# Kernel tuning notes

Measured on AMD Instinct MI355X. Metric: run time of the kernel, lower is better.

The kernel has to match this reference:

```python
import jax, jax.numpy as jnp
import numpy as np

N_MEL = 80; ARNN = 1024; ADIM = 128; EMB = 512; PRE = 256; DRNN = 1024; NF = 32; KS = 31
B = 32; NCTX = 512; T = 500
PAD = (KS - 1) // 2


def setup_inputs() -> dict:
    key = jax.random.key(0)
    ks = jax.random.split(key, 20)
    g = lambda k, shape: jax.random.normal(k, shape, dtype=jnp.float32) * 0.02
    return {
        "memory": jax.random.normal(ks[0], (B, NCTX, EMB), dtype=jnp.float32),
        "decoder_inputs": jax.random.normal(ks[1], (B, N_MEL, T), dtype=jnp.float32),
        "mask": jnp.zeros((B, NCTX), dtype=bool),
        "prenet_w1": g(ks[2], (PRE, N_MEL)),
        "prenet_w2": g(ks[3], (PRE, PRE)),
        "arnn_wih": g(ks[4], (4 * ARNN, PRE + EMB)),
        "arnn_whh": g(ks[5], (4 * ARNN, ARNN)),
        "arnn_bih": jnp.zeros((4 * ARNN,), jnp.float32),
        "arnn_bhh": jnp.zeros((4 * ARNN,), jnp.float32),
        "q_w": g(ks[6], (ADIM, ARNN)),
        "m_w": g(ks[7], (ADIM, EMB)),
        "loc_conv_w": g(ks[8], (NF, 2, KS)),
        "loc_w": g(ks[9], (ADIM, NF)),
        "v_w": g(ks[10], (ADIM,)),
        "drnn_wih": g(ks[11], (4 * DRNN, ARNN + EMB)),
        "drnn_whh": g(ks[12], (4 * DRNN, DRNN)),
        "drnn_bih": jnp.zeros((4 * DRNN,), jnp.float32),
        "drnn_bhh": jnp.zeros((4 * DRNN,), jnp.float32),
        "proj_w": g(ks[13], (N_MEL, DRNN + EMB)),
        "proj_b": jnp.zeros((N_MEL,), jnp.float32),
        "gate_w": g(ks[14], (1, DRNN + EMB)),
        "gate_b": jnp.zeros((1,), jnp.float32),
    }


def _lstm_cell(x, h, c, wih, whh, bih, bhh):
    # PyTorch LSTMCell gate order: i, f, g, o
    z = x @ wih.T + h @ whh.T + bih + bhh
    i, f, g, o = jnp.split(z, 4, axis=-1)
    c2 = jax.nn.sigmoid(f) * c + jax.nn.sigmoid(i) * jnp.tanh(g)
    h2 = jax.nn.sigmoid(o) * jnp.tanh(c2)
    return h2, c2


def reference(memory, decoder_inputs, mask,
              prenet_w1, prenet_w2,
              arnn_wih, arnn_whh, arnn_bih, arnn_bhh,
              q_w, m_w, loc_conv_w, loc_w, v_w,
              drnn_wih, drnn_whh, drnn_bih, drnn_bhh,
              proj_w, proj_b, gate_w, gate_b):
    b, n_ctx, emb = memory.shape
    n_mel, t_out = decoder_inputs.shape[1], decoder_inputs.shape[2]

    # (time, batch, n_mel) with a leading zero go-frame; PreNet (eval: no dropout)
    x = jnp.transpose(decoder_inputs, (2, 0, 1))
    x = jnp.concatenate([jnp.zeros((1, b, n_mel), x.dtype), x], axis=0)
    h = jax.nn.relu(x @ prenet_w1.T)
    h = jax.nn.relu(h @ prenet_w2.T)  # (T+1, B, PRE)
    inputs = h[:-1]  # T decoder steps

    proc_mem = memory @ m_w.T  # (B, n_ctx, ADIM)

    def step(carry, xin):
        ah, ac, dh, dc, aw, awc, actx = carry
        cell_in = jnp.concatenate([xin, actx], axis=-1)
        ah, ac = _lstm_cell(cell_in, ah, ac, arnn_wih, arnn_whh, arnn_bih, arnn_bhh)
        # location-sensitive attention
        aw_cat = jnp.stack([aw, awc], axis=1)  # (B, 2, n_ctx)
        loc = jax.lax.conv_general_dilated(
            aw_cat, loc_conv_w, window_strides=(1,), padding=[(PAD, PAD)],
            dimension_numbers=("NCH", "OIH", "NCH"))  # (B, NF, n_ctx)
        loc = jnp.transpose(loc, (0, 2, 1)) @ loc_w.T  # (B, n_ctx, ADIM)
        q = (ah @ q_w.T)[:, None, :]  # (B, 1, ADIM)
        e = jnp.tanh(q + proc_mem + loc) @ v_w  # (B, n_ctx)
        e = jnp.where(mask, -1e9, e)
        aw = jax.nn.softmax(e, axis=-1)
        actx = jnp.einsum("bn,bne->be", aw, memory)
        awc = awc + aw
        din = jnp.concatenate([ah, actx], axis=-1)
        dh, dc = _lstm_cell(din, dh, dc, drnn_wih, drnn_whh, drnn_bih, drnn_bhh)
        dhc = jnp.concatenate([dh, actx], axis=-1)
        mel = dhc @ proj_w.T + proj_b  # (B, n_mel)
        gate = dhc @ gate_w.T + gate_b  # (B, 1)
        return (ah, ac, dh, dc, aw, awc, actx), (mel, gate[:, 0])

    z32 = lambda *s: jnp.zeros(s, memory.dtype)
    carry0 = (z32(b, ARNN), z32(b, ARNN), z32(b, DRNN), z32(b, DRNN),
              z32(b, n_ctx), z32(b, n_ctx), z32(b, emb))
    _, (mels, gates) = jax.lax.scan(step, carry0, inputs)
    mel_out = jnp.transpose(mels, (1, 2, 0))   # (B, n_mel, T)
    gate_out = jnp.transpose(gates, (1, 0))    # (B, T)
    return mel_out, gate_out
```

## Files before the change

kernel.cpp:

```cpp
#include <hip/hip_runtime.h>

#define NBLK 256
#define NTHR 1024

constexpr int kNMel = 80, kArnn = 1024, kAdim = 128, kEmb = 512, kPre = 256;
constexpr int kNF = 32, kKS = 31, kB = 32, kNctx = 512, kT = 500, kPad = 15;

constexpr int KT_A = 56;
constexpr int KT_D = 80;
constexpr int KT_ALL = KT_A + KT_D;

constexpr int OFF_PREB   = 0;
constexpr int OFF_PROCMB = OFF_PREB + kT * kB * kPre / 2;
constexpr int OFF_QWTB   = OFF_PROCMB + kB * kNctx * kAdim / 2;
constexpr int OFF_LWT    = OFF_QWTB + kAdim * kArnn / 2;
constexpr int OFF_STATE  = OFF_LWT + kAdim * 33;
constexpr int OFF_AHB    = OFF_STATE;
constexpr int OFF_DHB    = OFF_AHB + 2 * kB * kArnn / 2;
constexpr int OFF_DH     = OFF_DHB + 2 * kB * kArnn / 2;
constexpr int OFF_AC     = OFF_DH + 2 * kB * kArnn;
constexpr int OFF_DC     = OFF_AC + kB * kArnn;
constexpr int OFF_ACTX   = OFF_DC + kB * kArnn;
constexpr int OFF_AW     = OFF_ACTX + kB * kEmb;
constexpr int OFF_AWC    = OFF_AW + kB * kNctx;
constexpr int OFF_PAW    = OFF_AWC + kB * kNctx;
constexpr int OFF_NUM    = OFF_PAW + kB * kNctx;
constexpr int OFF_DEN    = OFF_NUM + 2 * kB * kEmb;
constexpr int OFF_END    = OFF_DEN + 2 * kB;
constexpr int STATE_SZ   = OFF_END - OFF_STATE;
constexpr int OFF_BAR    = OFF_END;
constexpr int BAR_LINES  = 266;
constexpr int OFF_PAN    = OFF_BAR + BAR_LINES * 32;
constexpr int PAN_SZ     = NBLK * KT_ALL * 256;
constexpr int OFF_GMB    = OFF_PAN + PAN_SZ;
constexpr int GMB_SZ     = kB * kNctx * kEmb / 2;

typedef __attribute__((ext_vector_type(4))) float fvec4;
typedef __attribute__((ext_vector_type(8))) short bh8_t;
typedef unsigned long long u64;
typedef unsigned short ushortt;

union U64u { u64 u; float2 f2; ushortt s[4]; };

union SMem {
  struct { ushortt xs[16][2048]; } x1;
  struct { float zra[4][2][64][4]; float zrd[4][2][64][4];
           float hb[2][32][4]; } x2;
  struct { float ahb_s[kArnn]; float vw_s[kAdim]; float psum[1024]; float q_s[kAdim];
           float aw_s[96]; float awc_s[96]; float cw[kNF * 2 * kKS];
           float loc_s[64 * 33]; float p_s[64]; float lwt[kAdim * 33];
           float dhc[kArnn + kEmb]; float pprj[126];
           ushortt pm[64 * kAdim]; } b;
  struct { float x8[8][80]; float h1[8][256]; } p;
  struct { float mem_s[4][512]; } m;
};

__device__ __forceinline__ float sigf(float x) { return 1.0f / (1.0f + __expf(-x)); }
__device__ __forceinline__ float tanhfast(float x) { return 1.0f - 2.0f / (__expf(2.0f * x) + 1.0f); }

__device__ __forceinline__ ushortt bf16rn(float f) {
  unsigned u = __float_as_uint(f);
  unsigned r = (u + 0x7FFFu + ((u >> 16) & 1u)) >> 16;
  return (ushortt)r;
}
__device__ __forceinline__ float bf2f(ushortt v) {
  return __uint_as_float((unsigned)v << 16);
}

__device__ __forceinline__ u64 ald64(const void* p) {
  return __hip_atomic_load((const u64*)p, __ATOMIC_RELAXED, __HIP_MEMORY_SCOPE_AGENT);
}
__device__ __forceinline__ float alf(const float* p) {
  return __hip_atomic_load(p, __ATOMIC_RELAXED, __HIP_MEMORY_SCOPE_AGENT);
}
__device__ __forceinline__ void asf(float* p, float v) {
  __hip_atomic_store(p, v, __ATOMIC_RELAXED, __HIP_MEMORY_SCOPE_AGENT);
}
__device__ __forceinline__ void as64(void* p, u64 v) {
  __hip_atomic_store((u64*)p, v, __ATOMIC_RELAXED, __HIP_MEMORY_SCOPE_AGENT);
}
__device__ __forceinline__ unsigned alu(const unsigned* p) {
  return __hip_atomic_load(p, __ATOMIC_RELAXED, __HIP_MEMORY_SCOPE_AGENT);
}
__device__ __forceinline__ void asu(unsigned* p, unsigned v) {
  __hip_atomic_store(p, v, __ATOMIC_RELAXED, __HIP_MEMORY_SCOPE_AGENT);
}

__device__ __forceinline__ void gbar_full(unsigned* cnt, unsigned* gen, unsigned& genv) {
  __syncthreads();
  if (threadIdx.x == 0) {
    __threadfence();
    unsigned arrived = __hip_atomic_fetch_add(cnt, 1u, __ATOMIC_ACQ_REL, __HIP_MEMORY_SCOPE_AGENT) + 1u;
    if (arrived == (unsigned)NBLK) {
      __hip_atomic_store(cnt, 0u, __ATOMIC_RELAXED, __HIP_MEMORY_SCOPE_AGENT);
      __hip_atomic_fetch_add(gen, 1u, __ATOMIC_ACQ_REL, __HIP_MEMORY_SCOPE_AGENT);
    } else {
      while (__hip_atomic_load(gen, __ATOMIC_ACQUIRE, __HIP_MEMORY_SCOPE_AGENT) == genv) {
        __builtin_amdgcn_s_sleep(2);
      }
    }
    ++genv;
  }
  __syncthreads();
}

__device__ __forceinline__ void gbar_light(unsigned* bar, unsigned target, int bk, int tid) {
  asm volatile("s_waitcnt vmcnt(0) lgkmcnt(0)" ::: "memory");
  __syncthreads();
  if (bk == 0) {
    if (tid < 64) {
      if (tid == 0) asm volatile("s_waitcnt vmcnt(0)" ::: "memory");
      unsigned i0 = (unsigned)tid * 4, i1 = i0 + 1, i2 = i0 + 2, i3 = i0 + 3;
      for (;;) {
        bool ok = true;
        if (i0 != 0) ok = ok && (alu(&bar[i0 * 32]) >= target);
        ok = ok && (alu(&bar[i1 * 32]) >= target);
        ok = ok && (alu(&bar[i2 * 32]) >= target);
        ok = ok && (alu(&bar[i3 * 32]) >= target);
        if (__all(ok)) break;
        __builtin_amdgcn_s_sleep(1);
      }
      if (tid < 8) asu(&bar[(256 + tid) * 32], target);
    }
  } else {
    if (tid == 0) {
      asm volatile("s_waitcnt vmcnt(0)" ::: "memory");
      asu(&bar[bk * 32], target);
      unsigned* wk = &bar[(256 + (bk & 7)) * 32];
      while (alu(wk) < target) __builtin_amdgcn_s_sleep(1);
    }
  }
  __syncthreads();
}

template<int LS, int SL, int MH>
__device__ __forceinline__ void lstm_wave(
    const ushortt* __restrict__ s0, const ushortt* __restrict__ s2,
    const float* __restrict__ numq, const float* __restrict__ invden,
    const short* __restrict__ pan,
    int l, ushortt* xs, fvec4& z)
{
  constexpr int NC  = LS ? 10 : 7;
  constexpr int CB  = LS ? SL * 640 : SL * 448;
  constexpr int KT0 = LS ? SL * 20 : SL * 14;
  constexpr int BD0 = LS ? 1024 : 256;
  constexpr int BD1 = LS ? 1536 : 768;
  const int u8 = l & 15, rj = l >> 4;
  const int m = l & 15, kg = l >> 4;

  u64 L0[4], L1[4];
  bh8_t f00, f01, f10, f11;

  auto load = [&](int c, u64* L, bh8_t& f0, bh8_t& f1) {
    const int c0 = CB + c * 64;
    if (c0 >= BD0 && c0 < BD1) {
      const float* base = numq + (c0 - BD0) + u8 * 4;
      #pragma unroll
      for (int j = 0; j < 4; ++j) {
        int lr = 4 * j + rj;
        const float* fp = base + (size_t)(MH * 16 + lr) * kEmb;
        U64u a, b2; a.u = ald64(fp); b2.u = ald64(fp + 2);
        float s = invden[MH * 16 + lr];
        U64u pk;
        pk.s[0] = bf16rn(a.f2.x * s);  pk.s[1] = bf16rn(a.f2.y * s);
        pk.s[2] = bf16rn(b2.f2.x * s); pk.s[3] = bf16rn(b2.f2.y * s);
        L[j] = pk.u;
      }
    } else {
      const ushortt* bsrc; int stride; bool coh;
      if (c0 < BD0) { bsrc = s0 + c0;       stride = (LS ? 1024 : 256); coh = (LS == 1); }
      else          { bsrc = s2 + c0 - BD1; stride = 1024;              coh = true; }
      #pragma unroll
      for (int j = 0; j < 4; ++j) {
        const ushortt* ap = bsrc + (size_t)(MH * 16 + 4 * j + rj) * stride + u8 * 4;
        L[j] = coh ? ald64(ap) : *reinterpret_cast<const u64*>(ap);
      }
    }
    f0 = *reinterpret_cast<const bh8_t*>(pan + (size_t)(KT0 + c * 2) * 512 + l * 8);
    f1 = *reinterpret_cast<const bh8_t*>(pan + (size_t)(KT0 + c * 2 + 1) * 512 + l * 8);
  };
  auto stash = [&](int buf, u64* L) {
    #pragma unroll
    for (int j = 0; j < 4; ++j) {
      int lr = 4 * j + rj;
      int sw = u8 ^ ((lr & 7) << 1);
      *reinterpret_cast<u64*>(xs + buf * 1024 + lr * 64 + sw * 4) = L[j];
    }
  };
  auto consume = [&](int buf, bh8_t f0, bh8_t f1) {
    #pragma unroll
    for (int kt = 0; kt < 2; ++kt) {
      int sw = (2 * (kt * 4 + kg)) ^ ((m & 7) << 1);
      bh8_t a = *reinterpret_cast<const bh8_t*>(xs + buf * 1024 + m * 64 + sw * 4);
      z = __builtin_amdgcn_mfma_f32_16x16x32_bf16(a, kt ? f1 : f0, z, 0, 0, 0);
    }
  };

  load(0, L0, f00, f01);
  #pragma unroll
  for (int c = 0; c < NC; c += 2) {
    stash(0, L0);
    if (c + 1 < NC) load(c + 1, L1, f10, f11);
    consume(0, f00, f01);
    if (c + 1 < NC) {
      stash(1, L1);
      if (c + 2 < NC) load(c + 2, L0, f00, f01);
      consume(1, f10, f11);
    }
  }
}

extern "C" __global__ void __launch_bounds__(NTHR, 4)
decoder_kernel(const float* __restrict__ gmem, const float* __restrict__ dec,
               const unsigned char* __restrict__ mask,
               const float* __restrict__ pw1, const float* __restrict__ pw2,
               const float* __restrict__ awih, const float* __restrict__ awhh,
               const float* __restrict__ abih, const float* __restrict__ abhh,
               const float* __restrict__ qw, const float* __restrict__ mw,
               const float* __restrict__ cvw, const float* __restrict__ locw,
               const float* __restrict__ vw,
               const float* __restrict__ dwih, const float* __restrict__ dwhh,
               const float* __restrict__ dbih, const float* __restrict__ dbhh,
               const float* __restrict__ pjw, const float* __restrict__ pjb,
               const float* __restrict__ gw, const float* __restrict__ gb,
               float* __restrict__ out, float* __restrict__ ws, int useg)
{
  __shared__ SMem sm;
  __shared__ float s_invden[32];
  const int bk = blockIdx.x, tid = threadIdx.x;
  unsigned genv_f = 0, bcnt = 0;
  unsigned* bar = reinterpret_cast<unsigned*>(ws + OFF_BAR);
  unsigned* cntF = &bar[264 * 32];
  unsigned* genF = &bar[265 * 32];

  ushortt* PREBu = reinterpret_cast<ushortt*>(ws + OFF_PREB);
  ushortt* PROCMBu = reinterpret_cast<ushortt*>(ws + OFF_PROCMB);
  ushortt* QWTBu = reinterpret_cast<ushortt*>(ws + OFF_QWTB);
  float* LWT = ws + OFF_LWT;
  ushortt* AHBu = reinterpret_cast<ushortt*>(ws + OFF_AHB);
  ushortt* DHBu = reinterpret_cast<ushortt*>(ws + OFF_DHB);
  float* DH = ws + OFF_DH;
  float* AC = ws + OFF_AC;
  float* DC = ws + OFF_DC;
  float* ACTX = ws + OFF_ACTX;
  float* AWp = ws + OFF_AW;
  float* AWC = ws + OFF_AWC;
  float* PAW = ws + OFF_PAW;
  float* NUM = ws + OFF_NUM;
  float* DEN = ws + OFF_DEN;
  short* PANS = reinterpret_cast<short*>(ws + OFF_PAN);
  ushortt* GMB = reinterpret_cast<ushortt*>(ws + OFF_GMB);

  for (int i = bk * NTHR + tid; i < STATE_SZ; i += NBLK * NTHR) (ws + OFF_STATE)[i] = 0.f;
  for (int i = bk * NTHR + tid; i < kAdim * kArnn; i += NBLK * NTHR)
    QWTBu[i] = bf16rn(qw[i]);
  for (int i = bk * NTHR + tid; i < kAdim * kNF; i += NBLK * NTHR) {
    int d = i >> 5, f = i & 31;
    LWT[d * 33 + f] = locw[i];
  }
  gbar_full(cntF, genF, genv_f);

  if (bk == 0 && tid < 2 * kB) asf(&DEN[tid], 1.0f);
  for (int it = 0; it < 16; ++it) {
    int task0 = bk * 64 + it * 4;
    for (int i = tid; i < 2048; i += NTHR) {
      int pr = i >> 9, h = i & 511;
      sm.m.mem_s[pr][h] = gmem[(size_t)(task0 + pr) * kEmb + h];
    }
    __syncthreads();
    if (tid < 512) {
      int pr = tid >> 7, d = tid & 127;
      const float* mwr = mw + d * kEmb;
      float acc = 0.f;
      for (int h = 0; h < kEmb; ++h) acc = fmaf(sm.m.mem_s[pr][h], mwr[h], acc);
      PROCMBu[(size_t)(task0 + pr) * kAdim + d] = bf16rn(acc);
    }
    if (useg) {
      for (int i = tid; i < 2048; i += NTHR) {
        int pr = i >> 9, h = i & 511;
        GMB[(size_t)(task0 + pr) * kEmb + h] = bf16rn(sm.m.mem_s[pr][h]);
      }
    }
    __syncthreads();
  }
  for (int g = bk; g < 2000; g += NBLK) {
    int t_idx = g >> 2;
    int b0 = (g & 3) * 8;
    if (t_idx == 0) {
      for (int i = tid; i < 8 * kPre; i += NTHR)
        PREBu[(size_t)(b0 + (i >> 8)) * kPre + (i & 255)] = 0;
      continue;
    }
    for (int i = tid; i < 640; i += NTHR) {
      int bb = i / 80, m2 = i % 80;
      sm.p.x8[bb][m2] = dec[((size_t)(b0 + bb) * kNMel + m2) * kT + (t_idx - 1)];
    }
    __syncthreads();
    if (tid < 512) {
      int u = tid & 255, rep = tid >> 8;
      float acc[4] = {0.f, 0.f, 0.f, 0.f};
      for (int m2 = 0; m2 < 80; ++m2) {
        float w = pw1[u * kNMel + m2];
        #pragma unroll
        for (int r = 0; r < 4; ++r) acc[r] = fmaf(w, sm.p.x8[rep * 4 + r][m2], acc[r]);
      }
      #pragma unroll
      for (int r = 0; r < 4; ++r) sm.p.h1[rep * 4 + r][u] = fmaxf(acc[r], 0.f);
    }
    __syncthreads();
    if (tid < 512) {
      int u = tid & 255, rep = tid >> 8;
      float acc[4] = {0.f, 0.f, 0.f, 0.f};
      for (int k = 0; k < kPre; ++k) {
        float w = pw2[u * kPre + k];
        #pragma unroll
        for (int r = 0; r < 4; ++r) acc[r] = fmaf(w, sm.p.h1[rep * 4 + r][k], acc[r]);
      }
      #pragma unroll
      for (int r = 0; r < 4; ++r)
        PREBu[((size_t)t_idx * kB + b0 + rep * 4 + r) * kPre + u] = bf16rn(fmaxf(acc[r], 0.f));
    }
    __syncthreads();
  }
  {
    const int UNITS = NBLK * KT_ALL * 64;
    for (int u = bk * NTHR + tid; u < UNITS; u += NBLK * NTHR) {
      int bkk = u / (KT_ALL * 64);
      int rem = u - bkk * (KT_ALL * 64);
      int kta = rem >> 6, l = rem & 63;
      int lstm = (kta >= KT_A);
      int kt = lstm ? kta - KT_A : kta;
      int n = l & 15, kg = l >> 4;
      int r = (n >> 2) * 1024 + bkk * 4 + (n & 3);
      bh8_t v;
      #pragma unroll
      for (int j = 0; j < 8; ++j) {
        int k = kt * 32 + kg * 8 + j;
        float wv;
        if (!lstm) wv = (k < 768) ? awih[(size_t)r * 768 + k] : awhh[(size_t)r * 1024 + (k - 768)];
        else       wv = (k < 1536) ? dwih[(size_t)r * 1536 + k] : dwhh[(size_t)r * 1024 + (k - 1536)];
        v[j] = (short)bf16rn(wv);
      }
      *reinterpret_cast<bh8_t*>(PANS + (size_t)u * 8) = v;
    }
  }
  gbar_full(cntF, genF, genv_f);

  for (int t = 0; t <= kT; ++t) {
    const int p = t & 1, q = p ^ 1;
    float* nump = NUM + p * kB * kEmb;
    const float* numq = NUM + q * kB * kEmb;

    if (tid < kB) s_invden[tid] = 1.0f / alf(DEN + q * kB + tid);
    __syncthreads();
    if (t > 0 && tid < 64) {
      int idx = bk * 64 + tid;
      int b2 = idx >> 9;
      float invd = s_invden[b2];
      float av = PAW[idx] * invd;
      asf(&AWp[idx], av);
      asf(&AWC[idx], alf(&AWC[idx]) + av);
      asf(&ACTX[idx], alf(&numq[idx]) * invd);
    }
    if (t < kT) {
      if (tid < 64) asf(&nump[bk * 64 + tid], 0.f);
      if (bk == 0 && tid < kB) asf(DEN + p * kB + tid, 0.f);
    }
    {
      const int wid = tid >> 6, l = tid & 63;
      fvec4 z = {0.f, 0.f, 0.f, 0.f};
      const ushortt* AHBq_ = AHBu + q * kB * kArnn;
      const ushortt* DHBp_ = DHBu + p * kB * kArnn;
      const ushortt* preb_t = PREBu + (size_t)t * kB * kPre;
      ushortt* xs = &sm.x1.xs[wid][0];
      const short* panb = PANS + (size_t)bk * (KT_ALL * 512);
      const short* pand = panb + KT_A * 512;
      if (wid < 8) {
        if (t < kT) {
          switch (wid) {
            case 0: lstm_wave<0,0,0>(preb_t, AHBq_, numq, s_invden, panb, l, xs, z); break;
            case 1: lstm_wave<0,0,1>(preb_t, AHBq_, numq, s_invden, panb, l, xs, z); break;
            case 2: lstm_wave<0,1,0>(preb_t, AHBq_, numq, s_invden, panb, l, xs, z); break;
            case 3: lstm_wave<0,1,1>(preb_t, AHBq_, numq, s_invden, panb, l, xs, z); break;
            case 4: lstm_wave<0,2,0>(preb_t, AHBq_, numq, s_invden, panb, l, xs, z); break;
            case 5: lstm_wave<0,2,1>(preb_t, AHBq_, numq, s_invden, panb, l, xs, z); break;
            case 6: lstm_wave<0,3,0>(preb_t, AHBq_, numq, s_invden, panb, l, xs, z); break;
            default: lstm_wave<0,3,1>(preb_t, AHBq_, numq, s_invden, panb, l, xs, z); break;
          }
        }
      } else {
        if (t > 0) {
          switch (wid) {
            case 8:  lstm_wave<1,0,0>(AHBq_, DHBp_, numq, s_invden, pand, l, xs, z); break;
            case 9:  lstm_wave<1,0,1>(AHBq_, DHBp_, numq, s_invden, pand, l, xs, z); break;
            case 10: lstm_wave<1,1,0>(AHBq_, DHBp_, numq, s_invden, pand, l, xs, z); break;
            case 11: lstm_wave<1,1,1>(AHBq_, DHBp_, numq, s_invden, pand, l, xs, z); break;
            case 12: lstm_wave<1,2,0>(AHBq_, DHBp_, numq, s_invden, pand, l, xs, z); break;
            case 13: lstm_wave<1,2,1>(AHBq_, DHBp_, numq, s_invden, pand, l, xs, z); break;
            case 14: lstm_wave<1,3,0>(AHBq_, DHBp_, numq, s_invden, pand, l, xs, z); break;
            default: lstm_wave<1,3,1>(AHBq_, DHBp_, numq, s_invden, pand, l, xs, z); break;
          }
        }
      }
      __syncthreads();
      const int sl = (wid & 7) >> 1, mh = wid & 1;
      if (wid < 8) *reinterpret_cast<fvec4*>(&sm.x2.zra[sl][mh][l][0]) = z;
      else         *reinterpret_cast<fvec4*>(&sm.x2.zrd[sl][mh][l][0]) = z;
    }
    __syncthreads();
    if (tid < 256) {
      const int ls = tid >> 7, uu = (tid >> 5) & 3, b = tid & 31;
      const bool go = (ls == 0) ? (t < kT) : (t > 0);
      if (go) {
        const int mt = b >> 4, mm = b & 15;
        const int lane_base = (mm >> 2) * 16, rr = mm & 3;
        float zg[4];
        #pragma unroll
        for (int g = 0; g < 4; ++g) {
          int ln = lane_base + g * 4 + uu;
          float s;
          if (ls == 0)
            s = sm.x2.zra[0][mt][ln][rr] + sm.x2.zra[1][mt][ln][rr]
              + sm.x2.zra[2][mt][ln][rr] + sm.x2.zra[3][mt][ln][rr];
          else
            s = sm.x2.zrd[0][mt][ln][rr] + sm.x2.zrd[1][mt][ln][rr]
              + sm.x2.zrd[2][mt][ln][rr] + sm.x2.zrd[3][mt][ln][rr];
          int rg = g * 1024 + bk * 4 + uu;
          s += (ls ? dbih[rg] + dbhh[rg] : abih[rg] + abhh[rg]);
          zg[g] = s;
        }
        float* cst = ls ? DC : AC;
        const int idx = b * kArnn + bk * 4 + uu;
        float c = sigf(zg[1]) * cst[idx] + sigf(zg[0]) * tanhfast(zg[2]);
        cst[idx] = c;
        float h = sigf(zg[3]) * tanhfast(c);
        if (ls) asf(&DH[q * kB * kArnn + idx], h);
        sm.x2.hb[ls][b][uu] = h;
      }
    }
    __syncthreads();
    if (tid < 64) {
      int ls = tid >> 5, b = tid & 31;
      bool go2 = ls ? (t > 0) : (t < kT);
      if (go2) {
        U64u pk;
        #pragma unroll
        for (int j = 0; j < 4; ++j) pk.s[j] = bf16rn(sm.x2.hb[ls][b][j]);
        ushortt* dst = (ls ? (DHBu + q * kB * kArnn) : (AHBu + p * kB * kArnn)) + b * kArnn + bk * 4;
        as64(dst, pk.u);
      }
    }
    gbar_light(bar, ++bcnt, bk, tid);

    if (t < kT) {
      const int b = bk >> 3, sub = bk & 7, j0 = sub * 64;
      const int pbase = (sub == 0) ? 0 : 21 + (sub - 1) * 20;
      const int pcnt = (sub == 0) ? 21 : 20;
      const ushortt* AHBp_ = AHBu + p * kB * kArnn;
      if (tid < 256) {
        U64u v; v.u = ald64(AHBp_ + b * kArnn + tid * 4);
        #pragma unroll
        for (int j = 0; j < 4; ++j) sm.b.ahb_s[tid * 4 + j] = bf2f(v.s[j]);
      }
      for (int i = tid; i < 94; i += NTHR) {
        int jj = j0 - kPad + i;
        bool ok = (jj >= 0 && jj < kNctx);
        sm.b.aw_s[i] = ok ? alf(&AWp[b * kNctx + jj]) : 0.f;
        sm.b.awc_s[i] = ok ? alf(&AWC[b * kNctx + jj]) : 0.f;
      }
      for (int i = tid; i < kNF * 2 * kKS; i += NTHR) sm.b.cw[i] = cvw[i];
      for (int i = tid; i < kAdim * 33; i += NTHR) sm.b.lwt[i] = LWT[i];
      for (int i = tid; i < kAdim; i += NTHR) sm.b.vw_s[i] = vw[i];
      {
        const fvec4* src = reinterpret_cast<const fvec4*>(PROCMBu + (size_t)(b * kNctx + j0) * kAdim);
        fvec4* dst = reinterpret_cast<fvec4*>(sm.b.pm);
        for (int i = tid; i < 1024; i += NTHR) dst[i] = src[i];
      }
      if (sub < 4 && t > 0) {
        for (int i = tid; i < kArnn + kEmb; i += NTHR)
          sm.b.dhc[i] = (i < kArnn) ? alf(&DH[q * kB * kArnn + b * kArnn + i])
                                    : alf(&ACTX[b * kEmb + (i - kArnn)]);
      }
      __syncthreads();
      {
        int d = tid & 127, qr = tid >> 7;
        const ushortt* wq = QWTBu + (size_t)d * kArnn + qr * 128;
        const float* ahs = sm.b.ahb_s + qr * 128;
        float acc = 0.f;
        #pragma unroll 4
        for (int h8 = 0; h8 < 16; ++h8) {
          U64u a, c2;
          a.u = *reinterpret_cast<const u64*>(wq + h8 * 8);
          c2.u = *reinterpret_cast<const u64*>(wq + h8 * 8 + 4);
          #pragma unroll
          for (int j = 0; j < 4; ++j) acc = fmaf(bf2f(a.s[j]), ahs[h8 * 8 + j], acc);
          #pragma unroll
          for (int j = 0; j < 4; ++j) acc = fmaf(bf2f(c2.s[j]), ahs[h8 * 8 + 4 + j], acc);
        }
        sm.b.psum[tid] = acc;
      }
      __syncthreads();
      if (tid < kAdim) {
        float s = 0.f;
        #pragma unroll
        for (int k = 0; k < 8; ++k) s += sm.b.psum[tid + 128 * k];
        sm.b.q_s[tid] = s;
      }
      if (tid < 512) {
        int j = tid >> 3, f0 = (tid & 7) * 4;
        #pragma unroll
        for (int fi = 0; fi < 4; ++fi) {
          int f = f0 + fi;
          const float* w0 = &sm.b.cw[f * 62];
          float s = 0.f;
          for (int k = 0; k < kKS; ++k)
            s = fmaf(sm.b.aw_s[j + k], w0[k], fmaf(sm.b.awc_s[j + k], w0[31 + k], s));
          sm.b.loc_s[j * 33 + f] = s;
        }
      }
      if (sub < 4 && t > 0 && tid < pcnt * 6) {
        int ol = tid / 6, kc = tid % 6, og = pbase + ol;
        const float* row = (og < kNMel) ? pjw + (size_t)og * (kArnn + kEmb) : gw;
        const float* x = sm.b.dhc + kc * 256;
        const float* r2 = row + kc * 256;
        float acc = 0.f;
        for (int k = 0; k < 256; ++k) acc = fmaf(r2[k], x[k], acc);
        sm.b.pprj[tid] = acc;
      }
      __syncthreads();
      if (tid < 512) {
        int j = tid >> 3, grp = tid & 7, jj = j0 + j;
        float pe = 0.f;
        #pragma unroll 4
        for (int dd = 0; dd < 16; ++dd) {
          int d = grp + 8 * dd;
          float l2 = 0.f;
          const float* ls2 = &sm.b.loc_s[j * 33];
          const float* lw2 = &sm.b.lwt[d * 33];
          #pragma unroll 8
          for (int f = 0; f < kNF; ++f) l2 = fmaf(ls2[f], lw2[f], l2);
          float x = sm.b.q_s[d] + bf2f(sm.b.pm[j * kAdim + d]) + l2;
          pe = fmaf(sm.b.vw_s[d], tanhfast(x), pe);
        }
        pe += __shfl_xor(pe, 1);
        pe += __shfl_xor(pe, 2);
        pe += __shfl_xor(pe, 4);
        if (grp == 0) {
          float pv = mask[b * kNctx + jj] ? 0.f : __expf(pe);
          sm.b.p_s[j] = pv;
          PAW[b * kNctx + jj] = pv;
        }
      }
      if (sub < 4 && t > 0 && tid < pcnt) {
        int og = pbase + tid;
        float val = (og < kNMel) ? pjb[og] : gb[0];
        #pragma unroll
        for (int kc = 0; kc < 6; ++kc) val += sm.b.pprj[tid * 6 + kc];
        if (og < kNMel) out[((size_t)b * kNMel + og) * kT + (t - 1)] = val;
        else out[(size_t)kB * kNMel * kT + b * kT + (t - 1)] = val;
      }
      __syncthreads();
      if (tid < 64) {
        float v = sm.b.p_s[tid];
        #pragma unroll
        for (int o = 1; o < 64; o <<= 1) v += __shfl_xor(v, o);
        if (tid == 0) atomicAdd(DEN + p * kB + b, v);
      }
      {
        int col = tid & 511, half = tid >> 9;
        int jbase = half * 32;
        if (useg) {
          const ushortt* memb = GMB + (size_t)(b * kNctx + j0 + jbase) * kEmb + col;
          float a0 = 0.f, a1 = 0.f, a2 = 0.f, a3 = 0.f;
          #pragma unroll 4
          for (int jj2 = 0; jj2 < 32; jj2 += 4) {
            a0 = fmaf(sm.b.p_s[jbase + jj2],     bf2f(memb[(size_t)jj2 * kEmb]), a0);
            a1 = fmaf(sm.b.p_s[jbase + jj2 + 1], bf2f(memb[(size_t)(jj2 + 1) * kEmb]), a1);
            a2 = fmaf(sm.b.p_s[jbase + jj2 + 2], bf2f(memb[(size_t)(jj2 + 2) * kEmb]), a2);
            a3 = fmaf(sm.b.p_s[jbase + jj2 + 3], bf2f(memb[(size_t)(jj2 + 3) * kEmb]), a3);
          }
          atomicAdd(&nump[b * kEmb + col], (a0 + a1) + (a2 + a3));
        } else {
          const float* memb = gmem + (size_t)(b * kNctx + j0 + jbase) * kEmb + col;
          float a0 = 0.f, a1 = 0.f;
          #pragma unroll 8
          for (int jj2 = 0; jj2 < 32; jj2 += 2) {
            a0 = fmaf(sm.b.p_s[jbase + jj2], memb[(size_t)jj2 * kEmb], a0);
            a1 = fmaf(sm.b.p_s[jbase + jj2 + 1], memb[(size_t)(jj2 + 1) * kEmb], a1);
          }
          atomicAdd(&nump[b * kEmb + col], a0 + a1);
        }
      }
      gbar_light(bar, ++bcnt, bk, tid);
    }
  }

  if (bk < kB) {
    const int b = bk;
    for (int i = tid; i < kArnn + kEmb; i += NTHR)
      sm.b.dhc[i] = (i < kArnn) ? alf(&DH[1 * kB * kArnn + b * kArnn + i])
                                : alf(&ACTX[b * kEmb + (i - kArnn)]);
    __syncthreads();
    if (tid < 486) {
      int ol = tid / 6, kc = tid % 6;
      const float* row = (ol < kNMel) ? pjw + (size_t)ol * (kArnn + kEmb) : gw;
      const float* x = sm.b.dhc + kc * 256;
      const float* r2 = row + kc * 256;
      float acc = 0.f;
      for (int k = 0; k < 256; ++k) acc = fmaf(r2[k], x[k], acc);
      sm.b.psum[tid] = acc;
    }
    __syncthreads();
    if (tid < 81) {
      float val = (tid < kNMel) ? pjb[tid] : gb[0];
      #pragma unroll
      for (int kc = 0; kc < 6; ++kc) val += sm.b.psum[tid * 6 + kc];
      if (tid < kNMel) out[((size_t)b * kNMel + tid) * kT + (kT - 1)] = val;
      else out[(size_t)kB * kNMel * kT + b * kT + (kT - 1)] = val;
    }
  }
}

extern "C" void kernel_launch(void* const* d_in, const int* in_sizes, int n_in,
                              void* d_out, int out_size, void* d_ws, size_t ws_size,
                              hipStream_t stream) {
  const float* gmem = (const float*)d_in[0];
  const float* dec = (const float*)d_in[1];
  const unsigned char* mask = (const unsigned char*)d_in[2];
  const float* pw1 = (const float*)d_in[3];
  const float* pw2 = (const float*)d_in[4];
  const float* awih = (const float*)d_in[5];
  const float* awhh = (const float*)d_in[6];
  const float* abih = (const float*)d_in[7];
  const float* abhh = (const float*)d_in[8];
  const float* qw = (const float*)d_in[9];
  const float* mw = (const float*)d_in[10];
  const float* cvw = (const float*)d_in[11];
  const float* locw = (const float*)d_in[12];
  const float* vw = (const float*)d_in[13];
  const float* dwih = (const float*)d_in[14];
  const float* dwhh = (const float*)d_in[15];
  const float* dbih = (const float*)d_in[16];
  const float* dbhh = (const float*)d_in[17];
  const float* pjw = (const float*)d_in[18];
  const float* pjb = (const float*)d_in[19];
  const float* gw = (const float*)d_in[20];
  const float* gb = (const float*)d_in[21];
  float* out = (float*)d_out;
  float* ws = (float*)d_ws;

  int useg = (ws_size >= (size_t)(OFF_GMB + GMB_SZ) * sizeof(float)) ? 1 : 0;

  hipMemsetAsync((char*)d_ws + (size_t)OFF_BAR * sizeof(float), 0,
                 (size_t)BAR_LINES * 128, stream);
  hipLaunchKernelGGL(decoder_kernel, dim3(NBLK), dim3(NTHR), 0, stream,
                     gmem, dec, mask, pw1, pw2, awih, awhh, abih, abhh, qw, mw,
                     cvw, locw, vw, dwih, dwhh, dbih, dbhh, pjw, pjb, gw, gb,
                     out, ws, useg);
}
```

Before: 40.14 ms.

## Split LSTM GEMM along K across waves, each wave covering all batch rows

Each wave now computes both 16-row batch halves, using two MFMA accumulators per wave, over a narrower K slice. Before, each wave handled one batch half over a wider K range. The weight fragments are loaded once and reused for both halves, which halves the per-wave weight panel traffic and shortens each wave's serial MFMA chain. In exchange, the reduction now sums 8 partials instead of 4, the shared memory scratch doubles, and the load/compute double-buffering is dropped, so each chunk's loads are no longer overlapped with MFMAs.

```diff
diff --git a/kernel.cpp b/kernel.cpp
--- a/kernel.cpp
+++ b/kernel.cpp
@@ -44,7 +44,7 @@
 
 union SMem {
   struct { ushortt xs[16][2048]; } x1;
-  struct { float zra[4][2][64][4]; float zrd[4][2][64][4];
+  struct { float zra[8][2][64][4]; float zrd[8][2][64][4];
            float hb[2][32][4]; } x2;
   struct { float ahb_s[kArnn]; float vw_s[kAdim]; float psum[1024]; float q_s[kAdim];
            float aw_s[96]; float awc_s[96]; float cw[kNF * 2 * kKS];
@@ -133,34 +133,33 @@
   __syncthreads();
 }
 
-template<int LS, int SL, int MH>
+template<int LS, int W>
 __device__ __forceinline__ void lstm_wave(
     const ushortt* __restrict__ s0, const ushortt* __restrict__ s2,
     const float* __restrict__ numq, const float* __restrict__ invden,
     const short* __restrict__ pan,
-    int l, ushortt* xs, fvec4& z)
+    int l, ushortt* xs, fvec4& z0, fvec4& z1)
 {
-  constexpr int NC  = LS ? 10 : 7;
-  constexpr int CB  = LS ? SL * 640 : SL * 448;
-  constexpr int KT0 = LS ? SL * 20 : SL * 14;
+  constexpr int NC  = LS ? 5 : (W < 4 ? 4 : 3);
+  constexpr int CB  = LS ? W * 320 : (W < 4 ? W * 256 : 1024 + (W - 4) * 192);
+  constexpr int KT0 = CB / 32;
   constexpr int BD0 = LS ? 1024 : 256;
   constexpr int BD1 = LS ? 1536 : 768;
   const int u8 = l & 15, rj = l >> 4;
   const int m = l & 15, kg = l >> 4;
 
-  u64 L0[4], L1[4];
-  bh8_t f00, f01, f10, f11;
-
-  auto load = [&](int c, u64* L, bh8_t& f0, bh8_t& f1) {
+  #pragma unroll
+  for (int c = 0; c < NC; ++c) {
     const int c0 = CB + c * 64;
+    u64 L[8];
     if (c0 >= BD0 && c0 < BD1) {
       const float* base = numq + (c0 - BD0) + u8 * 4;
       #pragma unroll
-      for (int j = 0; j < 4; ++j) {
-        int lr = 4 * j + rj;
-        const float* fp = base + (size_t)(MH * 16 + lr) * kEmb;
+      for (int j = 0; j < 8; ++j) {
+        int row = 4 * j + rj;
+        const float* fp = base + (size_t)row * kEmb;
         U64u a, b2; a.u = ald64(fp); b2.u = ald64(fp + 2);
-        float s = invden[MH * 16 + lr];
+        float s = invden[row];
         U64u pk;
         pk.s[0] = bf16rn(a.f2.x * s);  pk.s[1] = bf16rn(a.f2.y * s);
         pk.s[2] = bf16rn(b2.f2.x * s); pk.s[3] = bf16rn(b2.f2.y * s);
@@ -171,41 +170,27 @@
       if (c0 < BD0) { bsrc = s0 + c0;       stride = (LS ? 1024 : 256); coh = (LS == 1); }
       else          { bsrc = s2 + c0 - BD1; stride = 1024;              coh = true; }
       #pragma unroll
-      for (int j = 0; j < 4; ++j) {
-        const ushortt* ap = bsrc + (size_t)(MH * 16 + 4 * j + rj) * stride + u8 * 4;
+      for (int j = 0; j < 8; ++j) {
+        const ushortt* ap = bsrc + (size_t)(4 * j + rj) * stride + u8 * 4;
         L[j] = coh ? ald64(ap) : *reinterpret_cast<const u64*>(ap);
       }
     }
-    f0 = *reinterpret_cast<const bh8_t*>(pan + (size_t)(KT0 + c * 2) * 512 + l * 8);
-    f1 = *reinterpret_cast<const bh8_t*>(pan + (size_t)(KT0 + c * 2 + 1) * 512 + l * 8);
-  };
-  auto stash = [&](int buf, u64* L) {
+    bh8_t f0 = *reinterpret_cast<const bh8_t*>(pan + (size_t)(KT0 + c * 2) * 512 + l * 8);
+    bh8_t f1 = *reinterpret_cast<const bh8_t*>(pan + (size_t)(KT0 + c * 2 + 1) * 512 + l * 8);
     #pragma unroll
-    for (int j = 0; j < 4; ++j) {
-      int lr = 4 * j + rj;
-      int sw = u8 ^ ((lr & 7) << 1);
-      *reinterpret_cast<u64*>(xs + buf * 1024 + lr * 64 + sw * 4) = L[j];
-    }
-  };
-  auto consume = [&](int buf, bh8_t f0, bh8_t f1) {
+    for (int j = 0; j < 8; ++j) {
+      int row = 4 * j + rj;
+      int sw = u8 ^ ((row & 7) << 1);
+      *reinterpret_cast<u64*>(xs + row * 64 + sw * 4) = L[j];
+    }
     #pragma unroll
     for (int kt = 0; kt < 2; ++kt) {
       int sw = (2 * (kt * 4 + kg)) ^ ((m & 7) << 1);
-      bh8_t a = *reinterpret_cast<const bh8_t*>(xs + buf * 1024 + m * 64 + sw * 4);
-      z = __builtin_amdgcn_mfma_f32_16x16x32_bf16(a, kt ? f1 : f0, z, 0, 0, 0);
-    }
-  };
-
-  load(0, L0, f00, f01);
-  #pragma unroll
-  for (int c = 0; c < NC; c += 2) {
-    stash(0, L0);
-    if (c + 1 < NC) load(c + 1, L1, f10, f11);
-    consume(0, f00, f01);
-    if (c + 1 < NC) {
-      stash(1, L1);
-      if (c + 2 < NC) load(c + 2, L0, f00, f01);
-      consume(1, f10, f11);
+      bh8_t a0 = *reinterpret_cast<const bh8_t*>(xs + m * 64 + sw * 4);
+      bh8_t a1 = *reinterpret_cast<const bh8_t*>(xs + (16 + m) * 64 + sw * 4);
+      bh8_t f = kt ? f1 : f0;
+      z0 = __builtin_amdgcn_mfma_f32_16x16x32_bf16(a0, f, z0, 0, 0, 0);
+      z1 = __builtin_amdgcn_mfma_f32_16x16x32_bf16(a1, f, z1, 0, 0, 0);
     }
   }
 }
@@ -368,7 +353,7 @@
     }
     {
       const int wid = tid >> 6, l = tid & 63;
-      fvec4 z = {0.f, 0.f, 0.f, 0.f};
+      fvec4 z0 = {0.f, 0.f, 0.f, 0.f}, z1 = z0;
       const ushortt* AHBq_ = AHBu + q * kB * kArnn;
       const ushortt* DHBp_ = DHBu + p * kB * kArnn;
       const ushortt* preb_t = PREBu + (size_t)t * kB * kPre;
@@ -378,34 +363,38 @@
       if (wid < 8) {
         if (t < kT) {
           switch (wid) {
-            case 0: lstm_wave<0,0,0>(preb_t, AHBq_, numq, s_invden, panb, l, xs, z); break;
-            case 1: lstm_wave<0,0,1>(preb_t, AHBq_, numq, s_invden, panb, l, xs, z); break;
-            case 2: lstm_wave<0,1,0>(preb_t, AHBq_, numq, s_invden, panb, l, xs, z); break;
-            case 3: lstm_wave<0,1,1>(preb_t, AHBq_, numq, s_invden, panb, l, xs, z); break;
-            case 4: lstm_wave<0,2,0>(preb_t, AHBq_, numq, s_invden, panb, l, xs, z); break;
-            case 5: lstm_wave<0,2,1>(preb_t, AHBq_, numq, s_invden, panb, l, xs, z); break;
-            case 6: lstm_wave<0,3,0>(preb_t, AHBq_, numq, s_invden, panb, l, xs, z); break;
-            default: lstm_wave<0,3,1>(preb_t, AHBq_, numq, s_invden, panb, l, xs, z); break;
+            case 0: lstm_wave<0,0>(preb_t, AHBq_, numq, s_invden, panb, l, xs, z0, z1); break;
+            case 1: lstm_wave<0,1>(preb_t, AHBq_, numq, s_invden, panb, l, xs, z0, z1); break;
+            case 2: lstm_wave<0,2>(preb_t, AHBq_, numq, s_invden, panb, l, xs, z0, z1); break;
+            case 3: lstm_wave<0,3>(preb_t, AHBq_, numq, s_invden, panb, l, xs, z0, z1); break;
+            case 4: lstm_wave<0,4>(preb_t, AHBq_, numq, s_invden, panb, l, xs, z0, z1); break;
+            case 5: lstm_wave<0,5>(preb_t, AHBq_, numq, s_invden, panb, l, xs, z0, z1); break;
+            case 6: lstm_wave<0,6>(preb_t, AHBq_, numq, s_invden, panb, l, xs, z0, z1); break;
+            default: lstm_wave<0,7>(preb_t, AHBq_, numq, s_invden, panb, l, xs, z0, z1); break;
           }
         }
       } else {
         if (t > 0) {
           switch (wid) {
-            case 8:  lstm_wave<1,0,0>(AHBq_, DHBp_, numq, s_invden, pand, l, xs, z); break;
-            case 9:  lstm_wave<1,0,1>(AHBq_, DHBp_, numq, s_invden, pand, l, xs, z); break;
-            case 10: lstm_wave<1,1,0>(AHBq_, DHBp_, numq, s_invden, pand, l, xs, z); break;
-            case 11: lstm_wave<1,1,1>(AHBq_, DHBp_, numq, s_invden, pand, l, xs, z); break;
-            case 12: lstm_wave<1,2,0>(AHBq_, DHBp_, numq, s_invden, pand, l, xs, z); break;
-            case 13: lstm_wave<1,2,1>(AHBq_, DHBp_, numq, s_invden, pand, l, xs, z); break;
-            case 14: lstm_wave<1,3,0>(AHBq_, DHBp_, numq, s_invden, pand, l, xs, z); break;
-            default: lstm_wave<1,3,1>(AHBq_, DHBp_, numq, s_invden, pand, l, xs, z); break;
+            case 8:  lstm_wave<1,0>(AHBq_, DHBp_, numq, s_invden, pand, l, xs, z0, z1); break;
+            case 9:  lstm_wave<1,1>(AHBq_, DHBp_, numq, s_invden, pand, l, xs, z0, z1); break;
+            case 10: lstm_wave<1,2>(AHBq_, DHBp_, numq, s_invden, pand, l, xs, z0, z1); break;
+            case 11: lstm_wave<1,3>(AHBq_, DHBp_, numq, s_invden, pand, l, xs, z0, z1); break;
+            case 12: lstm_wave<1,4>(AHBq_, DHBp_, numq, s_invden, pand, l, xs, z0, z1); break;
+            case 13: lstm_wave<1,5>(AHBq_, DHBp_, numq, s_invden, pand, l, xs, z0, z1); break;
+            case 14: lstm_wave<1,6>(AHBq_, DHBp_, numq, s_invden, pand, l, xs, z0, z1); break;
+            default: lstm_wave<1,7>(AHBq_, DHBp_, numq, s_invden, pand, l, xs, z0, z1); break;
           }
         }
       }
       __syncthreads();
-      const int sl = (wid & 7) >> 1, mh = wid & 1;
-      if (wid < 8) *reinterpret_cast<fvec4*>(&sm.x2.zra[sl][mh][l][0]) = z;
-      else         *reinterpret_cast<fvec4*>(&sm.x2.zrd[sl][mh][l][0]) = z;
+      if (wid < 8) {
+        *reinterpret_cast<fvec4*>(&sm.x2.zra[wid][0][l][0]) = z0;
+        *reinterpret_cast<fvec4*>(&sm.x2.zra[wid][1][l][0]) = z1;
+      } else {
+        *reinterpret_cast<fvec4*>(&sm.x2.zrd[wid - 8][0][l][0]) = z0;
+        *reinterpret_cast<fvec4*>(&sm.x2.zrd[wid - 8][1][l][0]) = z1;
+      }
     }
     __syncthreads();
     if (tid < 256) {
@@ -418,13 +407,14 @@
         #pragma unroll
         for (int g = 0; g < 4; ++g) {
           int ln = lane_base + g * 4 + uu;
-          float s;
-          if (ls == 0)
-            s = sm.x2.zra[0][mt][ln][rr] + sm.x2.zra[1][mt][ln][rr]
-              + sm.x2.zra[2][mt][ln][rr] + sm.x2.zra[3][mt][ln][rr];
-          else
-            s = sm.x2.zrd[0][mt][ln][rr] + sm.x2.zrd[1][mt][ln][rr]
-              + sm.x2.zrd[2][mt][ln][rr] + sm.x2.zrd[3][mt][ln][rr];
+          float s = 0.f;
+          if (ls == 0) {
+            #pragma unroll
+            for (int w = 0; w < 8; ++w) s += sm.x2.zra[w][mt][ln][rr];
+          } else {
+            #pragma unroll
+            for (int w = 0; w < 8; ++w) s += sm.x2.zrd[w][mt][ln][rr];
+          }
           int rg = g * 1024 + bk * 4 + uu;
           s += (ls ? dbih[rg] + dbhh[rg] : abih[rg] + abhh[rg]);
           zg[g] = s;
```

After: 43.28 ms. +7.8%, slower.
